# Kernel tuning notes

Hardware: AMD Instinct MI355X
Metric: run time of the kernel (lower is better)

## Reference

```python
import jax, jax.numpy as jnp
import numpy as np

B, C, H, W = 16, 512, 64, 64


def setup_inputs() -> dict:
    key = jax.random.key(0)
    ks = jax.random.split(key, 8)
    s = 1.0 / np.sqrt(C)  # fan-in scale like torch conv default
    return {
        "x": jax.random.normal(ks[0], (B, C, H, W), dtype=jnp.float32),
        "y": jax.random.normal(ks[1], (B, C), dtype=jnp.float32),
        "wq": jax.random.normal(ks[2], (C, C), dtype=jnp.float32) * s,
        "bq": jax.random.normal(ks[3], (C,), dtype=jnp.float32) * s,
        "wk": jax.random.normal(ks[4], (C, C), dtype=jnp.float32) * s,
        "bk": jax.random.normal(ks[5], (C,), dtype=jnp.float32) * s,
        "wv": jax.random.normal(ks[6], (C, C), dtype=jnp.float32) * s,
        "bv": jax.random.normal(ks[7], (C,), dtype=jnp.float32) * s,
        "gamma": jnp.ones((1,), dtype=jnp.float32),
    }


def _conv1x1_flat(inp_flat, w, b):
    # inp_flat: (B, C, N); 1x1 conv == per-pixel channel GEMM
    return jnp.einsum("oc,bcn->bon", w, inp_flat) + b[None, :, None]


def reference(x, y, wq, bq, wk, bk, wv, bv, gamma):
    b, c, h, w = x.shape
    n = h * w
    # align=True: y (B, C) broadcast to (B, C, H, W); flatten spatial dims
    y_flat = jnp.broadcast_to(y[:, :, None], (b, c, n))
    x_flat = x.reshape(b, c, n)
    # exchange=False: q = y, k = v = x
    pq = _conv1x1_flat(y_flat, wq, bq)          # (B, C, N)
    pk = _conv1x1_flat(x_flat, wk, bk)          # (B, C, N)
    pv = _conv1x1_flat(x_flat, wv, bv)          # (B, C, N)
    energy = jnp.einsum("bcn,bdn->bcd", pq, pk)  # (B, C, C) channel attention
    attn = jax.nn.softmax(energy, axis=-1)
    out = jnp.einsum("bcd,bdn->bcn", attn, pv)   # (B, C, N)
    out = out.reshape(b, c, h, w)
    return gamma * out + x
```

## Files before the change

kernel.cpp:

```cpp
#include <hip/hip_runtime.h>
#include <hip/hip_bf16.h>

#define Bn 16
#define Cn 512
#define Nn 4096

typedef unsigned short u16;
typedef __bf16 bf16x8 __attribute__((ext_vector_type(8)));
typedef float f32x4 __attribute__((ext_vector_type(4)));
typedef unsigned short u16x8 __attribute__((ext_vector_type(8)));

__device__ __forceinline__ u16 f2bf(float f) {
    __hip_bfloat16 h = __float2bfloat16(f);
    return *reinterpret_cast<u16*>(&h);
}

__device__ __forceinline__ void glds16(const u16* g, u16* l) {
    __builtin_amdgcn_global_load_lds(
        (const __attribute__((address_space(1))) void*)g,
        (__attribute__((address_space(3))) void*)l, 16, 0, 0);
}

__global__ __launch_bounds__(256) void k_transpose(
    const float* __restrict__ x, u16* __restrict__ xt, float* __restrict__ sxp)
{
    __shared__ float tile[128 * 65];
    const int b = blockIdx.z, c0 = blockIdx.y * 128, n0 = blockIdx.x * 64;
    const int t = threadIdx.x;
    const float* xb = x + ((size_t)(b * Cn + c0)) * Nn + n0;

    float part[8];
#pragma unroll
    for (int r = 0; r < 8; ++r) {
        int cl = (t >> 4) + r * 16;
        int nl = (t & 15) * 4;
        float4 v = *(const float4*)(xb + (size_t)cl * Nn + nl);
        float* tp = &tile[cl * 65 + nl];
        tp[0] = v.x; tp[1] = v.y; tp[2] = v.z; tp[3] = v.w;
        part[r] = (v.x + v.y) + (v.z + v.w);
    }
#pragma unroll
    for (int m = 1; m < 16; m <<= 1) {
#pragma unroll
        for (int r = 0; r < 8; ++r) part[r] += __shfl_xor(part[r], m);
    }
    if ((t & 15) == 0) {
#pragma unroll
        for (int r = 0; r < 8; ++r) {
            int cl = (t >> 4) + r * 16;
            sxp[(size_t)(b * Cn + c0 + cl) * 64 + blockIdx.x] = part[r];
        }
    }
    __syncthreads();
    u16* xtb = xt + ((size_t)(b * Nn + n0)) * Cn + c0;
#pragma unroll
    for (int r = 0; r < 4; ++r) {
        int nl = (t >> 4) + r * 16;
        int c8 = (t & 15) * 8;
        u16x8 hv;
#pragma unroll
        for (int i = 0; i < 8; ++i) hv[i] = f2bf(tile[(c8 + i) * 65 + nl]);
        *(u16x8*)(xtb + (size_t)nl * Cn + c8) = hv;
    }
}

__global__ __launch_bounds__(256) void k_sxred(
    const float* __restrict__ sxp, float* __restrict__ sx)
{
    int i = blockIdx.x * 256 + threadIdx.x;
    const float4* p = (const float4*)(sxp + (size_t)i * 64);
    float s = 0.f;
#pragma unroll
    for (int j = 0; j < 16; ++j) {
        float4 v = p[j];
        s += (v.x + v.y) + (v.z + v.w);
    }
    sx[i] = s;
}

__global__ __launch_bounds__(256) void k_qk(
    const float* __restrict__ wq, const float* __restrict__ bq,
    const float* __restrict__ wk, const float* __restrict__ bk,
    const float* __restrict__ y, const float* __restrict__ sx,
    float* __restrict__ qy, float* __restrict__ sk)
{
    const int w = threadIdx.x >> 6, lane = threadIdx.x & 63;
    const int o = blockIdx.x * 4 + w;
    const int b = blockIdx.y;
    const int mode = blockIdx.z;
    const float* W = mode ? wk : wq;
    const float* vec = mode ? (sx + b * Cn) : (y + b * Cn);
    float sum = 0.f;
#pragma unroll
    for (int i = 0; i < 8; ++i) {
        int k2 = lane + i * 64;
        sum += W[(size_t)o * Cn + k2] * vec[k2];
    }
#pragma unroll
    for (int m = 1; m < 64; m <<= 1) sum += __shfl_xor(sum, m);
    if (lane == 0) {
        if (mode) sk[b * Cn + o] = sum + 4096.0f * bk[o];
        else      qy[b * Cn + o] = sum + bq[o];
    }
}

__global__ __launch_bounds__(256) void k_wvt(
    const float* __restrict__ wv, u16* __restrict__ wvt)
{
    __shared__ float tl[64 * 65];
    const int d0 = blockIdx.x * 64, e0 = blockIdx.y * 64;
    const int t = threadIdx.x;
#pragma unroll
    for (int r = 0; r < 4; ++r) {
        int d = (t >> 4) + r * 16, e4 = (t & 15) * 4;
        float4 v = *(const float4*)(wv + (size_t)(d0 + d) * Cn + e0 + e4);
        float* p = &tl[d * 65 + e4];
        p[0] = v.x; p[1] = v.y; p[2] = v.z; p[3] = v.w;
    }
    __syncthreads();
#pragma unroll
    for (int r = 0; r < 4; ++r) {
        int e = (t >> 4) + r * 16, d4 = (t & 15) * 4;
        ushort4 h;
        h.x = f2bf(tl[(d4 + 0) * 65 + e]);
        h.y = f2bf(tl[(d4 + 1) * 65 + e]);
        h.z = f2bf(tl[(d4 + 2) * 65 + e]);
        h.w = f2bf(tl[(d4 + 3) * 65 + e]);
        *(ushort4*)(wvt + (size_t)(e0 + e) * Cn + d0 + d4) = h;
    }
}

__global__ __launch_bounds__(256) void k_softmax(
    const float* __restrict__ qy, const float* __restrict__ sk,
    const float* __restrict__ bv, u16* __restrict__ attn,
    float* __restrict__ beff)
{
    __shared__ float red[4], red2[4], red3[4];
    const int b = blockIdx.x >> 9, c = blockIdx.x & 511;
    const int t = threadIdx.x;
    const float q = qy[b * Cn + c];
    const float l0 = q * sk[b * Cn + t];
    const float l1 = q * sk[b * Cn + t + 256];
    float mx = fmaxf(l0, l1);
#pragma unroll
    for (int m = 1; m < 64; m <<= 1) mx = fmaxf(mx, __shfl_xor(mx, m));
    if ((t & 63) == 0) red[t >> 6] = mx;
    __syncthreads();
    mx = fmaxf(fmaxf(red[0], red[1]), fmaxf(red[2], red[3]));
    const float e0 = __expf(l0 - mx), e1 = __expf(l1 - mx);
    float s = e0 + e1;
#pragma unroll
    for (int m = 1; m < 64; m <<= 1) s += __shfl_xor(s, m);
    if ((t & 63) == 0) red2[t >> 6] = s;
    __syncthreads();
    s = red2[0] + red2[1] + red2[2] + red2[3];
    const float inv = 1.0f / s;
    const float a0 = e0 * inv, a1 = e1 * inv;
    u16* arow = attn + ((size_t)(b * Cn + c)) * Cn;
    arow[t] = f2bf(a0);
    arow[t + 256] = f2bf(a1);
    float pb = a0 * bv[t] + a1 * bv[t + 256];
#pragma unroll
    for (int m = 1; m < 64; m <<= 1) pb += __shfl_xor(pb, m);
    if ((t & 63) == 0) red3[t >> 6] = pb;
    __syncthreads();
    if (t == 0) beff[b * Cn + c] = red3[0] + red3[1] + red3[2] + red3[3];
}

template <int FINAL>
__global__ __launch_bounds__(256) void k_gemm(
    const u16* __restrict__ A, size_t strideA,
    const u16* __restrict__ Bt, size_t strideB,
    int N,
    u16* __restrict__ outBf, size_t strideOb,
    float* __restrict__ outF,
    const float* __restrict__ xres,
    const float* __restrict__ beff,
    const float* __restrict__ gamma)
{
    constexpr int K = 512;
    __shared__ float smem_f[8448];
    u16* la = (u16*)smem_f;
    u16* lb = la + 128 * 64;
    const int b = blockIdx.z;
    const int m0 = blockIdx.y * 128;
    const int n0 = blockIdx.x * 128;
    A  += (size_t)b * strideA;
    Bt += (size_t)b * strideB;
    const int t = threadIdx.x;
    const int lane = t & 63;
    const int w = t >> 6;
    const int wm = (w >> 1) * 64, wn = (w & 1) * 64;
    const int l15 = lane & 15, quad = lane >> 4;

    f32x4 acc[4][4];
#pragma unroll
    for (int i = 0; i < 4; ++i)
#pragma unroll
        for (int j = 0; j < 4; ++j)
            acc[i][j] = (f32x4){0.f, 0.f, 0.f, 0.f};

    const int srow8 = lane >> 3;
    const int lgcol = ((lane & 7) ^ srow8) * 8;

    for (int k0 = 0; k0 < K; k0 += 64) {
        __syncthreads();
#pragma unroll
        for (int j = 0; j < 4; ++j) {
            const int row = w * 32 + j * 8 + srow8;
            const int sb = (w * 256 + j * 64) * 8;
            glds16(A  + (size_t)(m0 + row) * K + k0 + lgcol, la + sb);
            glds16(Bt + (size_t)(n0 + row) * K + k0 + lgcol, lb + sb);
        }
        __syncthreads();

#pragma unroll
        for (int kk2 = 0; kk2 < 2; ++kk2) {
            bf16x8 af[4], bfr[4];
#pragma unroll
            for (int mi = 0; mi < 4; ++mi) {
                const int r = wm + mi * 16 + l15;
                const int pg = ((kk2 << 2) + quad) ^ (l15 & 7);
                af[mi] = *(const bf16x8*)&la[r * 64 + pg * 8];
            }
#pragma unroll
            for (int ni = 0; ni < 4; ++ni) {
                const int r = wn + ni * 16 + l15;
                const int pg = ((kk2 << 2) + quad) ^ (l15 & 7);
                bfr[ni] = *(const bf16x8*)&lb[r * 64 + pg * 8];
            }
#pragma unroll
            for (int mi = 0; mi < 4; ++mi)
#pragma unroll
                for (int ni = 0; ni < 4; ++ni)
                    acc[mi][ni] = __builtin_amdgcn_mfma_f32_16x16x32_bf16(
                        af[mi], bfr[ni], acc[mi][ni], 0, 0, 0);
        }
    }

    if (FINAL) {
        const float g = gamma[0];
        float* lc = smem_f;
#pragma unroll
        for (int h = 0; h < 2; ++h) {
            __syncthreads();
            if ((w >> 1) == h) {
#pragma unroll
                for (int mi = 0; mi < 4; ++mi)
#pragma unroll
                    for (int reg = 0; reg < 4; ++reg) {
                        const int rl = mi * 16 + quad * 4 + reg;
#pragma unroll
                        for (int ni = 0; ni < 4; ++ni)
                            lc[rl * 132 + wn + ni * 16 + l15] = acc[mi][ni][reg];
                    }
            }
            __syncthreads();
            const int rb = h * 64;
#pragma unroll
            for (int rr = 0; rr < 8; ++rr) {
                const int rl = rr * 8 + (t >> 5);
                const int c4 = (t & 31) * 4;
                float4 v = *(float4*)&lc[rl * 132 + c4];
                const int r = m0 + rb + rl;
                const float be = beff[b * Cn + r];
                const size_t base = ((size_t)(b * Cn + r)) * N + n0 + c4;
                float4 xr = *(const float4*)(xres + base);
                float4 o;
                o.x = g * (v.x + be) + xr.x;
                o.y = g * (v.y + be) + xr.y;
                o.z = g * (v.z + be) + xr.z;
                o.w = g * (v.w + be) + xr.w;
                *(float4*)(outF + base) = o;
            }
        }
    } else {
#pragma unroll
        for (int mi = 0; mi < 4; ++mi) {
#pragma unroll
            for (int reg = 0; reg < 4; ++reg) {
                const int r = m0 + wm + mi * 16 + quad * 4 + reg;
                const size_t base = (size_t)b * strideOb + (size_t)r * N;
#pragma unroll
                for (int ni = 0; ni < 4; ++ni) {
                    const int cidx = n0 + wn + ni * 16 + l15;
                    outBf[base + cidx] = f2bf(acc[mi][ni][reg]);
                }
            }
        }
    }
}

__global__ __launch_bounds__(512, 4) void k_gemm2(
    const u16* __restrict__ A,
    const u16* __restrict__ Bt,
    float* __restrict__ outF,
    const float* __restrict__ xres,
    const float* __restrict__ beff,
    const float* __restrict__ gamma)
{
    extern __shared__ u16 sm[];
    const int b = blockIdx.z;
    const int m0 = blockIdx.y << 8;
    const int n0 = blockIdx.x << 7;
    const int t = threadIdx.x;
    const int lane = t & 63, w = t >> 6;
    const int wm = (w >> 1) << 6, wn = (w & 1) << 6;
    const int l15 = lane & 15, quad = lane >> 4;

    const u16* Ag = A + (size_t)b * Cn * Cn;
    const u16* Bg = Bt + (size_t)b * ((size_t)Nn * Cn);
    const int srow = t >> 2;
    const int scol = (((t & 3) ^ ((srow >> 1) & 3))) << 3;
    const u16* pa = Ag + (size_t)(m0 + srow) * Cn + scol;
    const u16* pb = Bg + (size_t)(n0 + srow) * Cn + scol;
    u16* dw = sm + w * 512;

#define SLOTO(s) ((s) * 12288)
#define STGA(s, c, k0) \
    glds16(pa + (size_t)(c) * (128 * Cn) + (k0), dw + SLOTO(s) + (c) * 4096)
#define STGB(s, k0) glds16(pb + (k0), dw + SLOTO(s) + 8192)
#define FRG(base, row, qd) \
    (*(const bf16x8*)&sm[(base) + (row) * 32 + \
                         (((qd) ^ (((row) >> 1) & 3)) << 3)])

    f32x4 acc[4][4];
#pragma unroll
    for (int i = 0; i < 4; ++i)
#pragma unroll
        for (int j = 0; j < 4; ++j) acc[i][j] = (f32x4){0.f, 0.f, 0.f, 0.f};

    STGA(0, 0, 0); STGA(0, 1, 0); STGB(0, 0);
    STGA(1, 0, 32); STGA(1, 1, 32); STGB(1, 32);

#pragma unroll
    for (int tI = 0; tI < 16; ++tI) {
        if (tI < 15) { asm volatile("s_waitcnt vmcnt(3)" ::: "memory"); }
        else         { asm volatile("s_waitcnt vmcnt(0)" ::: "memory"); }
        __builtin_amdgcn_s_barrier();
        if (tI <= 13) {
            const int s2 = (tI + 2) % 3;
            const int k2 = (tI + 2) << 5;
            STGA(s2, 0, k2); STGA(s2, 1, k2); STGB(s2, k2);
        }
        const int sb = SLOTO(tI % 3);
        bf16x8 af[4], bf[4];
#pragma unroll
        for (int mi = 0; mi < 4; ++mi)
            af[mi] = FRG(sb, wm + mi * 16 + l15, quad);
#pragma unroll
        for (int ni = 0; ni < 4; ++ni)
            bf[ni] = FRG(sb + 8192, wn + ni * 16 + l15, quad);
        __builtin_amdgcn_s_setprio(1);
#pragma unroll
        for (int mi = 0; mi < 4; ++mi)
#pragma unroll
            for (int ni = 0; ni < 4; ++ni)
                acc[mi][ni] = __builtin_amdgcn_mfma_f32_16x16x32_bf16(
                    af[mi], bf[ni], acc[mi][ni], 0, 0, 0);
        __builtin_amdgcn_s_setprio(0);
    }
#undef STGA
#undef STGB
#undef FRG
#undef SLOTO

    __syncthreads();
    float* lc = (float*)sm;
    const float g = gamma[0];
#pragma unroll
    for (int h = 0; h < 4; ++h) {
        if (h) __syncthreads();
        if ((w >> 1) == h) {
#pragma unroll
            for (int mi = 0; mi < 4; ++mi)
#pragma unroll
                for (int reg = 0; reg < 4; ++reg) {
                    const int rl = mi * 16 + quad * 4 + reg;
#pragma unroll
                    for (int ni = 0; ni < 4; ++ni)
                        lc[rl * 132 + wn + ni * 16 + l15] = acc[mi][ni][reg];
                }
        }
        __syncthreads();
#pragma unroll
        for (int k = 0; k < 4; ++k) {
            const int r = (t >> 5) + k * 16;
            const int c4 = (t & 31) * 4;
            float4 v = *(float4*)&lc[r * 132 + c4];
            const int row = m0 + h * 64 + r;
            const float be = beff[b * Cn + row];
            const size_t base = ((size_t)(b * Cn + row)) * Nn + n0 + c4;
            float4 xr = *(const float4*)(xres + base);
            float4 o;
            o.x = g * (v.x + be) + xr.x;
            o.y = g * (v.y + be) + xr.y;
            o.z = g * (v.z + be) + xr.z;
            o.w = g * (v.w + be) + xr.w;
            *(float4*)(outF + base) = o;
        }
    }
}

extern "C" void kernel_launch(void* const* d_in, const int* in_sizes, int n_in,
                              void* d_out, int out_size, void* d_ws, size_t ws_size,
                              hipStream_t stream)
{
    const float* x     = (const float*)d_in[0];
    const float* y     = (const float*)d_in[1];
    const float* wq    = (const float*)d_in[2];
    const float* bq    = (const float*)d_in[3];
    const float* wk    = (const float*)d_in[4];
    const float* bk    = (const float*)d_in[5];
    const float* wv    = (const float*)d_in[6];
    const float* bv    = (const float*)d_in[7];
    const float* gamma = (const float*)d_in[8];
    float* out = (float*)d_out;

    char* ws = (char*)d_ws;
    u16*   xt   = (u16*)  (ws + 0);
    float* sxp  = (float*)(ws + 67108864);
    float* sx   = (float*)(ws + 69206016);
    float* qy   = (float*)(ws + 69238784);
    float* sk   = (float*)(ws + 69271552);
    float* beff = (float*)(ws + 69304320);
    u16*   attn = (u16*)  (ws + 69337088);
    u16*   wvt  = (u16*)  (ws + 77725696);
    u16*   weff = (u16*)  (ws + 78249984);

    k_transpose<<<dim3(64, 4, Bn), dim3(256), 0, stream>>>(x, xt, sxp);
    k_sxred<<<dim3(32), dim3(256), 0, stream>>>(sxp, sx);
    k_wvt<<<dim3(8, 8), dim3(256), 0, stream>>>(wv, wvt);
    k_qk<<<dim3(128, Bn, 2), dim3(256), 0, stream>>>(wq, bq, wk, bk, y, sx, qy, sk);
    k_softmax<<<dim3(Bn * Cn), dim3(256), 0, stream>>>(qy, sk, bv, attn, beff);
    k_gemm<0><<<dim3(4, 4, Bn), dim3(256), 0, stream>>>(
        attn, (size_t)Cn * Cn, wvt, (size_t)0, Cn,
        weff, (size_t)Cn * Cn, nullptr, nullptr, nullptr, nullptr);
    if (hipFuncSetAttribute((const void*)k_gemm2,
                            hipFuncAttributeMaxDynamicSharedMemorySize,
                            73728) == hipSuccess) {
        k_gemm2<<<dim3(Nn / 128, 2, Bn), dim3(512), 73728, stream>>>(
            weff, xt, out, x, beff, gamma);
    } else {
        k_gemm<1><<<dim3(32, 4, Bn), dim3(256), 0, stream>>>(
            weff, (size_t)Cn * Cn, xt, (size_t)Nn * Cn, Nn,
            nullptr, (size_t)0, out, x, beff, gamma);
    }
}
```

Before: 346.6 us.

## Remap gemm2 tiles per XCD and split A/B staging depths in pipeline

The block index is remapped so the blocks sharing an XCD work on adjacent N-tiles and both M-halves, which should improve L2 reuse of the activation tiles. The single 3-slot shared-memory ring is split into a 2-slot ring for the weight tile and a 5-slot ring for the activation tile, so B loads run four K-steps ahead and A loads run one ahead. Wait counts are adjusted to match. This is meant to hide global-load latency on the streamed activations, but A loads are now only one step ahead, which could expose their latency.

```diff
diff --git a/kernel.cpp b/kernel.cpp
--- a/kernel.cpp
+++ b/kernel.cpp
@@ -301,8 +301,10 @@
 {
     extern __shared__ u16 sm[];
     const int b = blockIdx.z;
-    const int m0 = blockIdx.y << 8;
-    const int n0 = blockIdx.x << 7;
+    const int f = blockIdx.x + (blockIdx.y << 5);
+    const int xcd = f & 7, sl = f >> 3;
+    const int m0 = (sl & 1) << 8;
+    const int n0 = ((xcd << 2) + (sl >> 1)) << 7;
     const int t = threadIdx.x;
     const int lane = t & 63, w = t >> 6;
     const int wm = (w >> 1) << 6, wn = (w & 1) << 6;
@@ -314,15 +316,18 @@
     const int scol = (((t & 3) ^ ((srow >> 1) & 3))) << 3;
     const u16* pa = Ag + (size_t)(m0 + srow) * Cn + scol;
     const u16* pb = Bg + (size_t)(n0 + srow) * Cn + scol;
-    u16* dw = sm + w * 512;
-
-#define SLOTO(s) ((s) * 12288)
+    const int dwo = w * 512;
+
 #define STGA(s, c, k0) \
-    glds16(pa + (size_t)(c) * (128 * Cn) + (k0), dw + SLOTO(s) + (c) * 4096)
-#define STGB(s, k0) glds16(pb + (k0), dw + SLOTO(s) + 8192)
-#define FRG(base, row, qd) \
-    (*(const bf16x8*)&sm[(base) + (row) * 32 + \
+    glds16(pa + (size_t)(c) * (128 * Cn) + (k0), \
+           sm + (s) * 8192 + (c) * 4096 + dwo)
+#define STGB(s, k0) glds16(pb + (k0), sm + 16384 + (s) * 4096 + dwo)
+#define FRGA(s, row, qd) \
+    (*(const bf16x8*)&sm[(s) * 8192 + (row) * 32 + \
                          (((qd) ^ (((row) >> 1) & 3)) << 3)])
+#define FRGB(s, row, qd) \
+    (*(const bf16x8*)&sm[16384 + (s) * 4096 + (row) * 32 + \
+                         (((qd) ^ (((row) >> 1) & 3)) << 3)])
 
     f32x4 acc[4][4];
 #pragma unroll
@@ -330,27 +335,30 @@
 #pragma unroll
         for (int j = 0; j < 4; ++j) acc[i][j] = (f32x4){0.f, 0.f, 0.f, 0.f};
 
-    STGA(0, 0, 0); STGA(0, 1, 0); STGB(0, 0);
-    STGA(1, 0, 32); STGA(1, 1, 32); STGB(1, 32);
+    STGA(0, 0, 0); STGA(0, 1, 0);
+    STGB(0, 0); STGB(1, 32); STGB(2, 64); STGB(3, 96);
 
 #pragma unroll
     for (int tI = 0; tI < 16; ++tI) {
-        if (tI < 15) { asm volatile("s_waitcnt vmcnt(3)" ::: "memory"); }
-        else         { asm volatile("s_waitcnt vmcnt(0)" ::: "memory"); }
+        if (tI == 0)       { asm volatile("s_waitcnt vmcnt(3)" ::: "memory"); }
+        else if (tI <= 12) { asm volatile("s_waitcnt vmcnt(1)" ::: "memory"); }
+        else               { asm volatile("s_waitcnt vmcnt(0)" ::: "memory"); }
         __builtin_amdgcn_s_barrier();
-        if (tI <= 13) {
-            const int s2 = (tI + 2) % 3;
-            const int k2 = (tI + 2) << 5;
-            STGA(s2, 0, k2); STGA(s2, 1, k2); STGB(s2, k2);
-        }
-        const int sb = SLOTO(tI % 3);
+        if (tI + 1 <= 15) {
+            STGA((tI + 1) & 1, 0, (tI + 1) << 5);
+            STGA((tI + 1) & 1, 1, (tI + 1) << 5);
+        }
+        if (tI + 4 <= 15) {
+            STGB((tI + 4) % 5, (tI + 4) << 5);
+        }
+        const int sa = tI & 1, sb5 = tI % 5;
         bf16x8 af[4], bf[4];
 #pragma unroll
         for (int mi = 0; mi < 4; ++mi)
-            af[mi] = FRG(sb, wm + mi * 16 + l15, quad);
+            af[mi] = FRGA(sa, wm + mi * 16 + l15, quad);
 #pragma unroll
         for (int ni = 0; ni < 4; ++ni)
-            bf[ni] = FRG(sb + 8192, wn + ni * 16 + l15, quad);
+            bf[ni] = FRGB(sb5, wn + ni * 16 + l15, quad);
         __builtin_amdgcn_s_setprio(1);
 #pragma unroll
         for (int mi = 0; mi < 4; ++mi)
@@ -362,8 +370,8 @@
     }
 #undef STGA
 #undef STGB
-#undef FRG
-#undef SLOTO
+#undef FRGA
+#undef FRGB
 
     __syncthreads();
     float* lc = (float*)sm;
@@ -439,7 +447,7 @@
     if (hipFuncSetAttribute((const void*)k_gemm2,
                             hipFuncAttributeMaxDynamicSharedMemorySize,
                             73728) == hipSuccess) {
-        k_gemm2<<<dim3(Nn / 128, 2, Bn), dim3(512), 73728, stream>>>(
+        k_gemm2<<<dim3(32, 2, Bn), dim3(512), 73728, stream>>>(
             weff, xt, out, x, beff, gamma);
     } else {
         k_gemm<1><<<dim3(32, 4, Bn), dim3(256), 0, stream>>>(
```

Measured after the change: 358.2 us. 1.03x slower.

## Fold gamma into weff/beff and preload residual into GEMM accumulators

Applied to the files above, without the earlier changes.

Gamma is folded into the effective weight matrix when weff is written, and into beff in the softmax kernel, so the final GEMM epilogue no longer multiplies by gamma. The final GEMM now seeds its MFMA accumulators with the residual x values before the K loop instead of reading x in the epilogue. This moves the residual read off the tail so it can overlap with the start of the pipeline, at the cost of strided scalar loads and extra register pressure early in the kernel. Gamma is applied before bf16 rounding, which slightly changes numerics.

```diff
diff --git a/kernel.cpp b/kernel.cpp
--- a/kernel.cpp
+++ b/kernel.cpp
@@ -133,7 +133,7 @@
 __global__ __launch_bounds__(256) void k_softmax(
     const float* __restrict__ qy, const float* __restrict__ sk,
     const float* __restrict__ bv, u16* __restrict__ attn,
-    float* __restrict__ beff)
+    float* __restrict__ beff, const float* __restrict__ gamma)
 {
     __shared__ float red[4], red2[4], red3[4];
     const int b = blockIdx.x >> 9, c = blockIdx.x & 511;
@@ -164,7 +164,8 @@
     for (int m = 1; m < 64; m <<= 1) pb += __shfl_xor(pb, m);
     if ((t & 63) == 0) red3[t >> 6] = pb;
     __syncthreads();
-    if (t == 0) beff[b * Cn + c] = red3[0] + red3[1] + red3[2] + red3[3];
+    if (t == 0)
+        beff[b * Cn + c] = gamma[0] * (red3[0] + red3[1] + red3[2] + red3[3]);
 }
 
 template <int FINAL>
@@ -239,7 +240,6 @@
     }
 
     if (FINAL) {
-        const float g = gamma[0];
         float* lc = smem_f;
 #pragma unroll
         for (int h = 0; h < 2; ++h) {
@@ -267,14 +267,15 @@
                 const size_t base = ((size_t)(b * Cn + r)) * N + n0 + c4;
                 float4 xr = *(const float4*)(xres + base);
                 float4 o;
-                o.x = g * (v.x + be) + xr.x;
-                o.y = g * (v.y + be) + xr.y;
-                o.z = g * (v.z + be) + xr.z;
-                o.w = g * (v.w + be) + xr.w;
+                o.x = (v.x + be) + xr.x;
+                o.y = (v.y + be) + xr.y;
+                o.z = (v.z + be) + xr.z;
+                o.w = (v.w + be) + xr.w;
                 *(float4*)(outF + base) = o;
             }
         }
     } else {
+        const float gs = gamma[0];
 #pragma unroll
         for (int mi = 0; mi < 4; ++mi) {
 #pragma unroll
@@ -284,7 +285,7 @@
 #pragma unroll
                 for (int ni = 0; ni < 4; ++ni) {
                     const int cidx = n0 + wn + ni * 16 + l15;
-                    outBf[base + cidx] = f2bf(acc[mi][ni][reg]);
+                    outBf[base + cidx] = f2bf(gs * acc[mi][ni][reg]);
                 }
             }
         }
@@ -296,8 +297,7 @@
     const u16* __restrict__ Bt,
     float* __restrict__ outF,
     const float* __restrict__ xres,
-    const float* __restrict__ beff,
-    const float* __restrict__ gamma)
+    const float* __restrict__ beff)
 {
     extern __shared__ u16 sm[];
     const int b = blockIdx.z;
@@ -326,9 +326,18 @@
 
     f32x4 acc[4][4];
 #pragma unroll
-    for (int i = 0; i < 4; ++i)
-#pragma unroll
-        for (int j = 0; j < 4; ++j) acc[i][j] = (f32x4){0.f, 0.f, 0.f, 0.f};
+    for (int mi = 0; mi < 4; ++mi)
+#pragma unroll
+        for (int reg = 0; reg < 4; ++reg) {
+            const int row = m0 + wm + mi * 16 + quad * 4 + reg;
+            const float* xr =
+                xres + ((size_t)(b * Cn + row)) * Nn + n0 + wn + l15;
+#pragma unroll
+            for (int ni = 0; ni < 4; ++ni)
+                acc[mi][ni][reg] = xr[ni * 16];
+        }
+    asm volatile("" ::: "memory");
+    __builtin_amdgcn_sched_barrier(0);
 
     STGA(0, 0, 0); STGA(0, 1, 0); STGB(0, 0);
     STGA(1, 0, 32); STGA(1, 1, 32); STGB(1, 32);
@@ -367,7 +376,6 @@
 
     __syncthreads();
     float* lc = (float*)sm;
-    const float g = gamma[0];
 #pragma unroll
     for (int h = 0; h < 4; ++h) {
         if (h) __syncthreads();
@@ -391,12 +399,11 @@
             const int row = m0 + h * 64 + r;
             const float be = beff[b * Cn + row];
             const size_t base = ((size_t)(b * Cn + row)) * Nn + n0 + c4;
-            float4 xr = *(const float4*)(xres + base);
             float4 o;
-            o.x = g * (v.x + be) + xr.x;
-            o.y = g * (v.y + be) + xr.y;
-            o.z = g * (v.z + be) + xr.z;
-            o.w = g * (v.w + be) + xr.w;
+            o.x = v.x + be;
+            o.y = v.y + be;
+            o.z = v.z + be;
+            o.w = v.w + be;
             *(float4*)(outF + base) = o;
         }
     }
@@ -432,15 +439,15 @@
     k_sxred<<<dim3(32), dim3(256), 0, stream>>>(sxp, sx);
     k_wvt<<<dim3(8, 8), dim3(256), 0, stream>>>(wv, wvt);
     k_qk<<<dim3(128, Bn, 2), dim3(256), 0, stream>>>(wq, bq, wk, bk, y, sx, qy, sk);
-    k_softmax<<<dim3(Bn * Cn), dim3(256), 0, stream>>>(qy, sk, bv, attn, beff);
+    k_softmax<<<dim3(Bn * Cn), dim3(256), 0, stream>>>(qy, sk, bv, attn, beff, gamma);
     k_gemm<0><<<dim3(4, 4, Bn), dim3(256), 0, stream>>>(
         attn, (size_t)Cn * Cn, wvt, (size_t)0, Cn,
-        weff, (size_t)Cn * Cn, nullptr, nullptr, nullptr, nullptr);
+        weff, (size_t)Cn * Cn, nullptr, nullptr, nullptr, gamma);
     if (hipFuncSetAttribute((const void*)k_gemm2,
                             hipFuncAttributeMaxDynamicSharedMemorySize,
                             73728) == hipSuccess) {
-        k_gemm2<<<dim3(Nn / 128, 2, Bn), dim3(512), 73728, stream>>>(
-            weff, xt, out, x, beff, gamma);
+        k_gemm2<<<dim3(32, 2, Bn), dim3(512), 73728, stream>>>(
+            weff, xt, out, x, beff);
     } else {
         k_gemm<1><<<dim3(32, 4, Bn), dim3(256), 0, stream>>>(
             weff, (size_t)Cn * Cn, xt, (size_t)Nn * Cn, Nn,
```

Result: no change. 353.4 us (+2.0%).
